# Kernel optimization log

Measured on AMD Instinct MI355X. Metric: run time of the kernel, lower is better.

The kernel has to match this reference:

```python
import jax, jax.numpy as jnp
import numpy as np

B, T, D, H, R = 16, 2048, 512, 1024, 16


def setup_inputs() -> dict:
    key = jax.random.key(0)
    ks = jax.random.split(key, 8)
    s = lambda d: 1.0 / np.sqrt(d)
    return {
        "x": jax.random.normal(ks[0], (B, T, D), jnp.float32),
        "Wx": jax.random.normal(ks[1], (D, H), jnp.float32) * s(D),
        "Wh": jax.random.normal(ks[2], (H, H), jnp.float32) * s(H),
        "Wq": jax.random.normal(ks[3], (D, R), jnp.float32) * s(D),
        "Wk": jax.random.normal(ks[4], (D, R), jnp.float32) * s(D),
        "Wv": jax.random.normal(ks[5], (D, H), jnp.float32) * s(D),
        "Wd": jax.random.normal(ks[6], (D, 1), jnp.float32) * s(D),
        "b": jnp.zeros((H,), jnp.float32),
        "bd": jnp.ones((1,), jnp.float32),
    }


def reference(x, Wx, Wh, Wq, Wk, Wv, Wd, b, bd):
    """DREAM fast-weight RNN.

    Per step: decay lambda_t = sigmoid(x_t Wd + bd)  (B,1)
              F_t = lambda_t * F_{t-1} + v_t k_t^T   (B,H,R) outer-product memory
              r_t = F_t q_t                          (B,H)   fast-weight read
              h_t = tanh(x_t Wx + h_{t-1} Wh + r_t + b)
    """
    Bsz = x.shape[0]
    Hd, Rk = Wv.shape[1], Wq.shape[1]
    # Precompute all time-parallel projections once (big GEMMs outside the scan).
    q = jnp.einsum('btd,dr->btr', x, Wq)            # (B,T,R)
    k = jnp.einsum('btd,dr->btr', x, Wk)            # (B,T,R)
    v = jnp.einsum('btd,dh->bth', x, Wv)            # (B,T,H)
    lam = jax.nn.sigmoid(jnp.einsum('btd,do->bto', x, Wd) + bd)  # (B,T,1)
    xw = jnp.einsum('btd,dh->bth', x, Wx)           # (B,T,H)

    h0 = jnp.zeros((Bsz, Hd), x.dtype)
    F0 = jnp.zeros((Bsz, Hd, Rk), x.dtype)

    def step(carry, inp):
        h, F = carry
        q_t, k_t, v_t, lam_t, xw_t = inp
        F = lam_t[:, :, None] * F + v_t[:, :, None] * k_t[:, None, :]  # (B,H,R)
        read = jnp.einsum('bhr,br->bh', F, q_t)
        h = jnp.tanh(xw_t + h @ Wh + read + b)
        return (h, F), h

    # scan over time axis
    inps = (q.transpose(1, 0, 2), k.transpose(1, 0, 2), v.transpose(1, 0, 2),
            lam.transpose(1, 0, 2), xw.transpose(1, 0, 2))
    (h_fin, F_fin), hs = jax.lax.scan(step, (h0, F0), inps)
    output = hs.transpose(1, 0, 2)  # (B,T,H)
    return output, h_fin, F_fin
```

## Files before the change

kernel.cpp:

```cpp
#include <hip/hip_runtime.h>
#include <math.h>

#define Bc 16
#define Tc 2048
#define Dc 512
#define Hc 1024
#define Rc 16

__global__ __launch_bounds__(256) void gemm_xw(const float* __restrict__ X,
                                               const float* __restrict__ W,
                                               float* __restrict__ out)
{
    __shared__ float As[16][128];
    __shared__ float Bs[16][64];
    const int tid = threadIdx.x;
    const int m0 = blockIdx.x * 128;
    const int n0 = blockIdx.y * 64;
    const int tx = tid & 15, ty = tid >> 4;
    const int am = tid >> 2, ak = (tid & 3) * 4;
    const int bk = tid >> 4, bn = (tid & 15) * 4;
    float acc[8][4] = {};
    for (int k0 = 0; k0 < 512; k0 += 16) {
        if (k0) __syncthreads();
        float4 a0 = *(const float4*)&X[(size_t)(m0 + am) * 512 + k0 + ak];
        float4 a1 = *(const float4*)&X[(size_t)(m0 + am + 64) * 512 + k0 + ak];
        float4 bv = *(const float4*)&W[(size_t)(k0 + bk) * 1024 + n0 + bn];
        As[ak + 0][am] = a0.x; As[ak + 1][am] = a0.y;
        As[ak + 2][am] = a0.z; As[ak + 3][am] = a0.w;
        As[ak + 0][am + 64] = a1.x; As[ak + 1][am + 64] = a1.y;
        As[ak + 2][am + 64] = a1.z; As[ak + 3][am + 64] = a1.w;
        *(float4*)&Bs[bk][bn] = bv;
        __syncthreads();
        #pragma unroll
        for (int kk = 0; kk < 16; ++kk) {
            float4 x0 = *(const float4*)&As[kk][ty * 8];
            float4 x1 = *(const float4*)&As[kk][ty * 8 + 4];
            float4 y  = *(const float4*)&Bs[kk][tx * 4];
            float a[8] = {x0.x, x0.y, x0.z, x0.w, x1.x, x1.y, x1.z, x1.w};
            float bb[4] = {y.x, y.y, y.z, y.w};
            #pragma unroll
            for (int i = 0; i < 8; ++i)
                #pragma unroll
                for (int j = 0; j < 4; ++j)
                    acc[i][j] += a[i] * bb[j];
        }
    }
    #pragma unroll
    for (int i = 0; i < 8; ++i) {
        float4 r;
        r.x = acc[i][0]; r.y = acc[i][1]; r.z = acc[i][2]; r.w = acc[i][3];
        *(float4*)&out[(size_t)(m0 + ty * 8 + i) * 1024 + n0 + tx * 4] = r;
    }
}

__global__ __launch_bounds__(256) void qkl_kernel(const float* __restrict__ X,
    const float* __restrict__ Wq, const float* __restrict__ Wk,
    const float* __restrict__ Wd, const float* __restrict__ bd,
    float* __restrict__ q, float* __restrict__ k, float* __restrict__ lam)
{
    __shared__ float xs[8 * 512];
    const int tid = threadIdx.x;
    const size_t row0 = (size_t)blockIdx.x * 8;
    #pragma unroll
    for (int c = 0; c < 4; ++c) {
        int f = (c * 256 + tid) * 4;
        *(float4*)&xs[f] = *(const float4*)&X[row0 * 512 + f];
    }
    __syncthreads();
    for (int t = tid; t < 264; t += 256) {
        int r = t / 33, c = t - r * 33;
        const float* xr = &xs[r * 512];
        const float* Wp; int ldw;
        if (c < 16)      { Wp = Wq + c;        ldw = 16; }
        else if (c < 32) { Wp = Wk + (c - 16); ldw = 16; }
        else             { Wp = Wd;            ldw = 1;  }
        float s = 0.f;
        for (int kk = 0; kk < 512; ++kk) s += xr[kk] * Wp[(size_t)kk * ldw];
        if (c < 16)      q[(row0 + r) * 16 + c] = s;
        else if (c < 32) k[(row0 + r) * 16 + (c - 16)] = s;
        else             lam[row0 + r] = 1.f / (1.f + expf(-(s + bd[0])));
    }
}

__global__ __launch_bounds__(256, 1) void rec_fused(
    const float* __restrict__ Wh, const float* __restrict__ qg,
    const float* __restrict__ kg, const float* __restrict__ vg,
    const float* __restrict__ lamg, const float* __restrict__ bias,
    float* __restrict__ out0, float* __restrict__ hfin,
    float* __restrict__ Ffin, float* __restrict__ hbuf)
{
    __shared__ float hs[4 * 1280];
    __shared__ float red2[2][256];
    __shared__ float pre_lds[2][64];
    __shared__ float F_lds[64][17];

    const int tid = threadIdx.x;
    const int w = blockIdx.x;
    const int sl = w & 63, g = w >> 6;
    const int c0 = sl * 16;
    const int kp = tid >> 2;
    const int cg = tid & 3;
    const int wv = tid >> 6;

    float wr[64];
    #pragma unroll
    for (int i = 0; i < 16; ++i) {
        float4 w4 = *(const float4*)&Wh[(size_t)(kp * 16 + i) * 1024 + c0 + cg * 4];
        wr[i * 4 + 0] = w4.x; wr[i * 4 + 1] = w4.y;
        wr[i * 4 + 2] = w4.z; wr[i * 4 + 3] = w4.w;
    }

    const int j64 = tid & 63;
    const int sb = j64 >> 4, scol = j64 & 15;
    const int sbg = g * 4 + sb;
    const bool isScan = (tid >= 192);
    const bool isFin  = (tid < 64);
    float bias_r = 0.f;
    float4 pq[4], pk4[4];
    float plam = 0.f, pv = 0.f, pxw = 0.f;
    if (isScan) {
        bias_r = bias[c0 + scol];
        #pragma unroll
        for (int r = 0; r < 16; ++r) F_lds[j64][r] = 0.f;
        const size_t row = (size_t)sbg * Tc;
        plam = lamg[row];
        pv   = vg[row * Hc + c0 + scol];
        pxw  = out0[row * Hc + c0 + scol];
        const float* qp = qg + row * 16;
        const float* kpp = kg + row * 16;
        #pragma unroll
        for (int r4 = 0; r4 < 4; ++r4) {
            pq[r4]  = *(const float4*)(qp + r4 * 4);
            pk4[r4] = *(const float4*)(kpp + r4 * 4);
        }
    }

    for (int t = 0; t < Tc; ++t) {
        const int buf = t & 1;
        float* h_rd = hbuf + (t & 1) * (Bc * Hc) + g * 4096;
        float* h_wr = hbuf + ((t + 1) & 1) * (Bc * Hc) + g * 4096;
        const float off_r = ((t >> 1) & 1) ? 4.0f : 0.0f;
        const float off_w = (((t + 1) >> 1) & 1) ? 4.0f : 0.0f;

        if (isScan) {
            float rd = 0.f;
            #pragma unroll
            for (int r4 = 0; r4 < 4; ++r4) {
                float f0 = F_lds[j64][r4 * 4 + 0];
                float f1 = F_lds[j64][r4 * 4 + 1];
                float f2 = F_lds[j64][r4 * 4 + 2];
                float f3 = F_lds[j64][r4 * 4 + 3];
                f0 = plam * f0 + pv * pk4[r4].x; rd += f0 * pq[r4].x;
                f1 = plam * f1 + pv * pk4[r4].y; rd += f1 * pq[r4].y;
                f2 = plam * f2 + pv * pk4[r4].z; rd += f2 * pq[r4].z;
                f3 = plam * f3 + pv * pk4[r4].w; rd += f3 * pq[r4].w;
                F_lds[j64][r4 * 4 + 0] = f0;
                F_lds[j64][r4 * 4 + 1] = f1;
                F_lds[j64][r4 * 4 + 2] = f2;
                F_lds[j64][r4 * 4 + 3] = f3;
            }
            pre_lds[buf][j64] = pxw + rd + bias_r;
            if (t == Tc - 1) {
                #pragma unroll
                for (int r = 0; r < 16; ++r)
                    Ffin[((size_t)sbg * Hc + c0 + scol) * 16 + r] = F_lds[j64][r];
            } else {
                const size_t row = (size_t)sbg * Tc + (t + 1);
                plam = lamg[row];
                pv   = vg[row * Hc + c0 + scol];
                pxw  = out0[row * Hc + c0 + scol];
                const float* qp = qg + row * 16;
                const float* kpp = kg + row * 16;
                #pragma unroll
                for (int r4 = 0; r4 < 4; ++r4) {
                    pq[r4]  = *(const float4*)(qp + r4 * 4);
                    pk4[r4] = *(const float4*)(kpp + r4 * 4);
                }
            }
        }

        {
            const int chunk = tid >> 2, coff = (tid & 3) * 4;
            float* base = &hs[chunk * 20 + coff];
            if (t > 0) {
                const float lo = off_r - 1.5f, hi = off_r + 1.5f;
                const float* p0 = h_rd + tid * 4;
                const float* p1 = p0 + 1024;
                const float* p2 = p0 + 2048;
                const float* p3 = p0 + 3072;
                float4 r0, r1, r2, r3;
                while (1) {
                    asm volatile(
                        "global_load_dwordx4 %0, %4, off sc0 sc1\n\t"
                        "global_load_dwordx4 %1, %5, off sc0 sc1\n\t"
                        "global_load_dwordx4 %2, %6, off sc0 sc1\n\t"
                        "global_load_dwordx4 %3, %7, off sc0 sc1\n\t"
                        "s_waitcnt vmcnt(0)"
                        : "=&v"(r0), "=&v"(r1), "=&v"(r2), "=&v"(r3)
                        : "v"(p0), "v"(p1), "v"(p2), "v"(p3)
                        : "memory");
                    bool ok = r0.x > lo && r0.x < hi && r0.y > lo && r0.y < hi
                           && r0.z > lo && r0.z < hi && r0.w > lo && r0.w < hi
                           && r1.x > lo && r1.x < hi && r1.y > lo && r1.y < hi
                           && r1.z > lo && r1.z < hi && r1.w > lo && r1.w < hi
                           && r2.x > lo && r2.x < hi && r2.y > lo && r2.y < hi
                           && r2.z > lo && r2.z < hi && r2.w > lo && r2.w < hi
                           && r3.x > lo && r3.x < hi && r3.y > lo && r3.y < hi
                           && r3.z > lo && r3.z < hi && r3.w > lo && r3.w < hi;
                    if (ok) break;
                }
                r0.x -= off_r; r0.y -= off_r; r0.z -= off_r; r0.w -= off_r;
                r1.x -= off_r; r1.y -= off_r; r1.z -= off_r; r1.w -= off_r;
                r2.x -= off_r; r2.y -= off_r; r2.z -= off_r; r2.w -= off_r;
                r3.x -= off_r; r3.y -= off_r; r3.z -= off_r; r3.w -= off_r;
                *(float4*)(base + 0 * 1280) = r0;
                *(float4*)(base + 1 * 1280) = r1;
                *(float4*)(base + 2 * 1280) = r2;
                *(float4*)(base + 3 * 1280) = r3;
            } else {
                float4 z = {0.f, 0.f, 0.f, 0.f};
                *(float4*)(base + 0 * 1280) = z;
                *(float4*)(base + 1 * 1280) = z;
                *(float4*)(base + 2 * 1280) = z;
                *(float4*)(base + 3 * 1280) = z;
            }
        }
        __syncthreads();

        float acc[16];
        #pragma unroll
        for (int z = 0; z < 16; ++z) acc[z] = 0.f;
        #pragma unroll
        for (int b = 0; b < 4; ++b) {
            const float* hb = &hs[b * 1280 + kp * 20];
            #pragma unroll
            for (int e = 0; e < 4; ++e) {
                float4 h4 = *(const float4*)(hb + e * 4);
                #pragma unroll
                for (int j = 0; j < 4; ++j)
                    acc[j * 4 + b] += h4.x * wr[(e * 4 + 0) * 4 + j]
                                    + h4.y * wr[(e * 4 + 1) * 4 + j]
                                    + h4.z * wr[(e * 4 + 2) * 4 + j]
                                    + h4.w * wr[(e * 4 + 3) * 4 + j];
            }
        }

        #pragma unroll
        for (int z = 0; z < 16; ++z) {
            float s = acc[z];
            s += __shfl_xor(s, 4);
            s += __shfl_xor(s, 8);
            s += __shfl_xor(s, 16);
            s += __shfl_xor(s, 32);
            acc[z] = s;
        }
        if (j64 < 4) {
            #pragma unroll
            for (int j = 0; j < 4; ++j) {
                float4 r4;
                r4.x = acc[j * 4 + 0]; r4.y = acc[j * 4 + 1];
                r4.z = acc[j * 4 + 2]; r4.w = acc[j * 4 + 3];
                *(float4*)&red2[buf][wv * 64 + (j64 * 4 + j) * 4] = r4;
            }
        }
        __syncthreads();

        if (isFin) {
            const int fb = tid >> 4, fcol = tid & 15;
            float tot = pre_lds[buf][tid];
            #pragma unroll
            for (int ww = 0; ww < 4; ++ww)
                tot += red2[buf][ww * 64 + fcol * 4 + fb];
            float hv = tanhf(tot);
            float sv = hv + off_w;
            float* hp = h_wr + fb * 1024 + c0 + fcol;
            asm volatile(
                "global_store_dword %0, %1, off sc0 sc1"
                :: "v"(hp), "v"(sv) : "memory");
            size_t oidx = ((size_t)(g * 4 + fb) * Tc + t) * Hc + c0 + fcol;
            out0[oidx] = hv;
            if (t == Tc - 1) hfin[(size_t)(g * 4 + fb) * Hc + c0 + fcol] = hv;
        }
    }
}

extern "C" void kernel_launch(void* const* d_in, const int* in_sizes, int n_in,
                              void* d_out, int out_size, void* d_ws, size_t ws_size,
                              hipStream_t stream)
{
    const float* x    = (const float*)d_in[0];
    const float* Wx   = (const float*)d_in[1];
    const float* Wh   = (const float*)d_in[2];
    const float* Wq   = (const float*)d_in[3];
    const float* Wk   = (const float*)d_in[4];
    const float* Wv   = (const float*)d_in[5];
    const float* Wd   = (const float*)d_in[6];
    const float* bias = (const float*)d_in[7];
    const float* bd   = (const float*)d_in[8];

    float* out0 = (float*)d_out;
    float* hfin = out0 + (size_t)Bc * Tc * Hc;
    float* Ffin = hfin + (size_t)Bc * Hc;

    float* wsf  = (float*)d_ws;
    float* v    = wsf;
    float* q    = v + (size_t)Bc * Tc * Hc;
    float* k    = q + (size_t)Bc * Tc * Rc;
    float* lam  = k + (size_t)Bc * Tc * Rc;
    float* hbuf = lam + (size_t)Bc * Tc;

    hipMemsetAsync(hbuf, 0x7F, 2 * (size_t)Bc * Hc * sizeof(float), stream);

    dim3 gg(256, 16);
    gemm_xw<<<gg, 256, 0, stream>>>(x, Wx, out0);
    gemm_xw<<<gg, 256, 0, stream>>>(x, Wv, v);
    qkl_kernel<<<4096, 256, 0, stream>>>(x, Wq, Wk, Wd, bd, q, k, lam);
    rec_fused<<<256, 256, 0, stream>>>(Wh, q, k, v, lam, bias,
                                       out0, hfin, Ffin, hbuf);
}
```

Before: 8.838 ms.

## Add a dedicated fifth wavefront for fast-weight scan and finalize, keep F in registers

The recurrent kernel grows from 256 to 320 threads per block. A separate fifth wavefront now runs the fast-weight memory update, the read, the tanh finalize and the global h store. The four compute wavefronts only do the h·Wh matvec. The F state moves from LDS into per-thread registers, and the pre-activation is passed in a register instead of through LDS. This removes the scan and finalize work from the matvec wavefronts and drops LDS traffic for F, which should shorten the per-step critical path. In exchange the block has one more wave to synchronise, and the finalize now runs on the same wave as the next step's scan, which could serialise them.

```diff
diff --git a/kernel.cpp b/kernel.cpp
--- a/kernel.cpp
+++ b/kernel.cpp
@@ -82,7 +82,7 @@
     }
 }
 
-__global__ __launch_bounds__(256, 1) void rec_fused(
+__global__ __launch_bounds__(320, 1) void rec_fused(
     const float* __restrict__ Wh, const float* __restrict__ qg,
     const float* __restrict__ kg, const float* __restrict__ vg,
     const float* __restrict__ lamg, const float* __restrict__ bias,
@@ -91,42 +91,45 @@
 {
     __shared__ float hs[4 * 1280];
     __shared__ float red2[2][256];
-    __shared__ float pre_lds[2][64];
-    __shared__ float F_lds[64][17];
 
     const int tid = threadIdx.x;
     const int w = blockIdx.x;
     const int sl = w & 63, g = w >> 6;
     const int c0 = sl * 16;
-    const int kp = tid >> 2;
+    const bool isC = (tid < 256);
+    const bool isS = (tid >= 256);
+    const int kp = (tid >> 2) & 63;
     const int cg = tid & 3;
     const int wv = tid >> 6;
+    const int j64 = tid & 63;
+    const int sb = j64 >> 4, scol = j64 & 15;
+    const int sbg = g * 4 + sb;
 
     float wr[64];
     #pragma unroll
     for (int i = 0; i < 16; ++i) {
-        float4 w4 = *(const float4*)&Wh[(size_t)(kp * 16 + i) * 1024 + c0 + cg * 4];
-        wr[i * 4 + 0] = w4.x; wr[i * 4 + 1] = w4.y;
-        wr[i * 4 + 2] = w4.z; wr[i * 4 + 3] = w4.w;
-    }
-
-    const int j64 = tid & 63;
-    const int sb = j64 >> 4, scol = j64 & 15;
-    const int sbg = g * 4 + sb;
-    const bool isScan = (tid >= 192);
-    const bool isFin  = (tid < 64);
-    float bias_r = 0.f;
+        if (isC) {
+            float4 w4 = *(const float4*)&Wh[(size_t)(kp * 16 + i) * 1024 + c0 + cg * 4];
+            wr[i * 4 + 0] = w4.x; wr[i * 4 + 1] = w4.y;
+            wr[i * 4 + 2] = w4.z; wr[i * 4 + 3] = w4.w;
+        } else {
+            wr[i * 4 + 0] = 0.f; wr[i * 4 + 1] = 0.f;
+            wr[i * 4 + 2] = 0.f; wr[i * 4 + 3] = 0.f;
+        }
+    }
+
+    float F[16];
+    #pragma unroll
+    for (int r = 0; r < 16; ++r) F[r] = 0.f;
+    float bias_r = 0.f, plam = 0.f, pv = 0.f, pxw = 0.f;
     float4 pq[4], pk4[4];
-    float plam = 0.f, pv = 0.f, pxw = 0.f;
-    if (isScan) {
+    if (isS) {
         bias_r = bias[c0 + scol];
-        #pragma unroll
-        for (int r = 0; r < 16; ++r) F_lds[j64][r] = 0.f;
         const size_t row = (size_t)sbg * Tc;
         plam = lamg[row];
         pv   = vg[row * Hc + c0 + scol];
         pxw  = out0[row * Hc + c0 + scol];
-        const float* qp = qg + row * 16;
+        const float* qp  = qg + row * 16;
         const float* kpp = kg + row * 16;
         #pragma unroll
         for (int r4 = 0; r4 < 4; ++r4) {
@@ -142,34 +145,31 @@
         const float off_r = ((t >> 1) & 1) ? 4.0f : 0.0f;
         const float off_w = (((t + 1) >> 1) & 1) ? 4.0f : 0.0f;
 
-        if (isScan) {
+        float pre_val = 0.f;
+        if (isS) {
             float rd = 0.f;
             #pragma unroll
             for (int r4 = 0; r4 < 4; ++r4) {
-                float f0 = F_lds[j64][r4 * 4 + 0];
-                float f1 = F_lds[j64][r4 * 4 + 1];
-                float f2 = F_lds[j64][r4 * 4 + 2];
-                float f3 = F_lds[j64][r4 * 4 + 3];
+                float f0 = F[r4 * 4 + 0], f1 = F[r4 * 4 + 1];
+                float f2 = F[r4 * 4 + 2], f3 = F[r4 * 4 + 3];
                 f0 = plam * f0 + pv * pk4[r4].x; rd += f0 * pq[r4].x;
                 f1 = plam * f1 + pv * pk4[r4].y; rd += f1 * pq[r4].y;
                 f2 = plam * f2 + pv * pk4[r4].z; rd += f2 * pq[r4].z;
                 f3 = plam * f3 + pv * pk4[r4].w; rd += f3 * pq[r4].w;
-                F_lds[j64][r4 * 4 + 0] = f0;
-                F_lds[j64][r4 * 4 + 1] = f1;
-                F_lds[j64][r4 * 4 + 2] = f2;
-                F_lds[j64][r4 * 4 + 3] = f3;
-            }
-            pre_lds[buf][j64] = pxw + rd + bias_r;
+                F[r4 * 4 + 0] = f0; F[r4 * 4 + 1] = f1;
+                F[r4 * 4 + 2] = f2; F[r4 * 4 + 3] = f3;
+            }
+            pre_val = pxw + rd + bias_r;
             if (t == Tc - 1) {
                 #pragma unroll
                 for (int r = 0; r < 16; ++r)
-                    Ffin[((size_t)sbg * Hc + c0 + scol) * 16 + r] = F_lds[j64][r];
+                    Ffin[((size_t)sbg * Hc + c0 + scol) * 16 + r] = F[r];
             } else {
                 const size_t row = (size_t)sbg * Tc + (t + 1);
                 plam = lamg[row];
                 pv   = vg[row * Hc + c0 + scol];
                 pxw  = out0[row * Hc + c0 + scol];
-                const float* qp = qg + row * 16;
+                const float* qp  = qg + row * 16;
                 const float* kpp = kg + row * 16;
                 #pragma unroll
                 for (int r4 = 0; r4 < 4; ++r4) {
@@ -179,7 +179,7 @@
             }
         }
 
-        {
+        if (isC) {
             const int chunk = tid >> 2, coff = (tid & 3) * 4;
             float* base = &hs[chunk * 20 + coff];
             if (t > 0) {
@@ -227,59 +227,59 @@
         }
         __syncthreads();
 
-        float acc[16];
-        #pragma unroll
-        for (int z = 0; z < 16; ++z) acc[z] = 0.f;
-        #pragma unroll
-        for (int b = 0; b < 4; ++b) {
-            const float* hb = &hs[b * 1280 + kp * 20];
-            #pragma unroll
-            for (int e = 0; e < 4; ++e) {
-                float4 h4 = *(const float4*)(hb + e * 4);
-                #pragma unroll
-                for (int j = 0; j < 4; ++j)
-                    acc[j * 4 + b] += h4.x * wr[(e * 4 + 0) * 4 + j]
-                                    + h4.y * wr[(e * 4 + 1) * 4 + j]
-                                    + h4.z * wr[(e * 4 + 2) * 4 + j]
-                                    + h4.w * wr[(e * 4 + 3) * 4 + j];
-            }
-        }
-
-        #pragma unroll
-        for (int z = 0; z < 16; ++z) {
-            float s = acc[z];
-            s += __shfl_xor(s, 4);
-            s += __shfl_xor(s, 8);
-            s += __shfl_xor(s, 16);
-            s += __shfl_xor(s, 32);
-            acc[z] = s;
-        }
-        if (j64 < 4) {
-            #pragma unroll
-            for (int j = 0; j < 4; ++j) {
-                float4 r4;
-                r4.x = acc[j * 4 + 0]; r4.y = acc[j * 4 + 1];
-                r4.z = acc[j * 4 + 2]; r4.w = acc[j * 4 + 3];
-                *(float4*)&red2[buf][wv * 64 + (j64 * 4 + j) * 4] = r4;
+        if (isC) {
+            float acc[16];
+            #pragma unroll
+            for (int z = 0; z < 16; ++z) acc[z] = 0.f;
+            #pragma unroll
+            for (int b = 0; b < 4; ++b) {
+                const float* hb = &hs[b * 1280 + kp * 20];
+                #pragma unroll
+                for (int e = 0; e < 4; ++e) {
+                    float4 h4 = *(const float4*)(hb + e * 4);
+                    #pragma unroll
+                    for (int j = 0; j < 4; ++j)
+                        acc[j * 4 + b] += h4.x * wr[(e * 4 + 0) * 4 + j]
+                                        + h4.y * wr[(e * 4 + 1) * 4 + j]
+                                        + h4.z * wr[(e * 4 + 2) * 4 + j]
+                                        + h4.w * wr[(e * 4 + 3) * 4 + j];
+                }
+            }
+            #pragma unroll
+            for (int z = 0; z < 16; ++z) {
+                float s = acc[z];
+                s += __shfl_xor(s, 4);
+                s += __shfl_xor(s, 8);
+                s += __shfl_xor(s, 16);
+                s += __shfl_xor(s, 32);
+                acc[z] = s;
+            }
+            if (j64 < 4) {
+                #pragma unroll
+                for (int j = 0; j < 4; ++j) {
+                    float4 r4;
+                    r4.x = acc[j * 4 + 0]; r4.y = acc[j * 4 + 1];
+                    r4.z = acc[j * 4 + 2]; r4.w = acc[j * 4 + 3];
+                    *(float4*)&red2[buf][wv * 64 + (j64 * 4 + j) * 4] = r4;
+                }
             }
         }
         __syncthreads();
 
-        if (isFin) {
-            const int fb = tid >> 4, fcol = tid & 15;
-            float tot = pre_lds[buf][tid];
+        if (isS) {
+            float tot = pre_val;
             #pragma unroll
             for (int ww = 0; ww < 4; ++ww)
-                tot += red2[buf][ww * 64 + fcol * 4 + fb];
+                tot += red2[buf][ww * 64 + scol * 4 + sb];
             float hv = tanhf(tot);
             float sv = hv + off_w;
-            float* hp = h_wr + fb * 1024 + c0 + fcol;
+            float* hp = h_wr + sb * 1024 + c0 + scol;
             asm volatile(
                 "global_store_dword %0, %1, off sc0 sc1"
                 :: "v"(hp), "v"(sv) : "memory");
-            size_t oidx = ((size_t)(g * 4 + fb) * Tc + t) * Hc + c0 + fcol;
+            size_t oidx = ((size_t)sbg * Tc + t) * Hc + c0 + scol;
             out0[oidx] = hv;
-            if (t == Tc - 1) hfin[(size_t)(g * 4 + fb) * Hc + c0 + fcol] = hv;
+            if (t == Tc - 1) hfin[(size_t)sbg * Hc + c0 + scol] = hv;
         }
     }
 }
@@ -315,6 +315,6 @@
     gemm_xw<<<gg, 256, 0, stream>>>(x, Wx, out0);
     gemm_xw<<<gg, 256, 0, stream>>>(x, Wv, v);
     qkl_kernel<<<4096, 256, 0, stream>>>(x, Wq, Wk, Wd, bd, q, k, lam);
-    rec_fused<<<256, 256, 0, stream>>>(Wh, q, k, v, lam, bias,
+    rec_fused<<<256, 320, 0, stream>>>(Wh, q, k, v, lam, bias,
                                        out0, hfin, Ffin, hbuf);
 }
```

Measured after the change: 13.03 ms. 1.47x slower.

## Repartition recurrence into 8 batch groups and add XCC-aware cache-coherent polling

Applied to the files above, without the earlier changes.

The recurrence is regrouped into 8 groups of 2 batches with 32 columns per block, where it was 4 groups of 4 batches with 16 columns. Each block now holds 128 Wh registers per thread and reads only 2 batch rows of h per step. Each block records which XCC it runs on in a table. When the producer block of a chunk is on the same XCC, the consumer polls with sc0-only loads to avoid system-level coherent traffic, and falls back to sc0 sc1 after 64 failed tries. This risks higher register pressure and depends on the reported XCC id being correct for L2-level coherence.

```diff
diff --git a/kernel.cpp b/kernel.cpp
--- a/kernel.cpp
+++ b/kernel.cpp
@@ -87,46 +87,73 @@
     const float* __restrict__ kg, const float* __restrict__ vg,
     const float* __restrict__ lamg, const float* __restrict__ bias,
     float* __restrict__ out0, float* __restrict__ hfin,
-    float* __restrict__ Ffin, float* __restrict__ hbuf)
+    float* __restrict__ Ffin, float* __restrict__ hbuf,
+    int* __restrict__ xcc_tab)
 {
-    __shared__ float hs[4 * 1280];
+    __shared__ float hs[2 * 1152];
     __shared__ float red2[2][256];
     __shared__ float pre_lds[2][64];
     __shared__ float F_lds[64][17];
 
     const int tid = threadIdx.x;
-    const int w = blockIdx.x;
-    const int sl = w & 63, g = w >> 6;
-    const int c0 = sl * 16;
-    const int kp = tid >> 2;
-    const int cg = tid & 3;
+    const int bid = blockIdx.x;
+    const int g = bid & 7, sl = bid >> 3;
+    const int c0 = sl * 32;
+    const int kp = tid >> 3;
+    const int cu = tid & 7;
     const int wv = tid >> 6;
 
-    float wr[64];
+    const int my_xcc = __builtin_amdgcn_s_getreg(63508) & 0xF;
+    if (tid == 0) {
+        int val = my_xcc + 1;
+        int* tp = xcc_tab + bid;
+        asm volatile("global_store_dword %0, %1, off sc0 sc1"
+                     :: "v"(tp), "v"(val) : "memory");
+    }
+
+    float wr[128];
     #pragma unroll
-    for (int i = 0; i < 16; ++i) {
-        float4 w4 = *(const float4*)&Wh[(size_t)(kp * 16 + i) * 1024 + c0 + cg * 4];
+    for (int i = 0; i < 32; ++i) {
+        float4 w4 = *(const float4*)&Wh[(size_t)(kp * 32 + i) * 1024 + c0 + cu * 4];
         wr[i * 4 + 0] = w4.x; wr[i * 4 + 1] = w4.y;
         wr[i * 4 + 2] = w4.z; wr[i * 4 + 3] = w4.w;
     }
 
+    const int sb_ = tid >> 7;
+    const int f   = (tid & 127) * 8;
+    float* stage_base = &hs[sb_ * 1152 + (f >> 5) * 36 + (f & 31)];
+
+    int fastf;
+    {
+        const int prod_bid = (f >> 5) * 8 + g;
+        const int* tp = xcc_tab + prod_bid;
+        int tv;
+        for (;;) {
+            asm volatile("global_load_dword %0, %1, off sc0 sc1\n\t"
+                         "s_waitcnt vmcnt(0)"
+                         : "=&v"(tv) : "v"(tp) : "memory");
+            if (tv != -1) break;
+        }
+        fastf = ((tv - 1) == my_xcc) ? 1 : 0;
+    }
+
     const int j64 = tid & 63;
-    const int sb = j64 >> 4, scol = j64 & 15;
-    const int sbg = g * 4 + sb;
+    const int fb = j64 >> 5, fci = j64 & 31;
+    const int bg = g * 2 + fb;
     const bool isScan = (tid >= 192);
     const bool isFin  = (tid < 64);
-    float bias_r = 0.f;
+
+    float bias_r = 0.f, plam = 0.f, pv = 0.f, pxw = 0.f;
     float4 pq[4], pk4[4];
-    float plam = 0.f, pv = 0.f, pxw = 0.f;
     if (isScan) {
-        bias_r = bias[c0 + scol];
+        bias_r = bias[c0 + fci];
         #pragma unroll
         for (int r = 0; r < 16; ++r) F_lds[j64][r] = 0.f;
-        const size_t row = (size_t)sbg * Tc;
+        const size_t row = (size_t)bg * Tc;
         plam = lamg[row];
-        pv   = vg[row * Hc + c0 + scol];
-        pxw  = out0[row * Hc + c0 + scol];
-        const float* qp = qg + row * 16;
+        pv   = vg[row * Hc + c0 + fci];
+        pxw  = out0[row * Hc + c0 + fci];
+        const float* qp  = qg + row * 16;
         const float* kpp = kg + row * 16;
         #pragma unroll
         for (int r4 = 0; r4 < 4; ++r4) {
@@ -137,8 +164,8 @@
 
     for (int t = 0; t < Tc; ++t) {
         const int buf = t & 1;
-        float* h_rd = hbuf + (t & 1) * (Bc * Hc) + g * 4096;
-        float* h_wr = hbuf + ((t + 1) & 1) * (Bc * Hc) + g * 4096;
+        float* h_rd = hbuf + (t & 1) * (16 * 1024) + g * 2048;
+        float* h_wr = hbuf + ((t + 1) & 1) * (16 * 1024) + g * 2048;
         const float off_r = ((t >> 1) & 1) ? 4.0f : 0.0f;
         const float off_w = (((t + 1) >> 1) & 1) ? 4.0f : 0.0f;
 
@@ -163,13 +190,13 @@
             if (t == Tc - 1) {
                 #pragma unroll
                 for (int r = 0; r < 16; ++r)
-                    Ffin[((size_t)sbg * Hc + c0 + scol) * 16 + r] = F_lds[j64][r];
+                    Ffin[((size_t)bg * Hc + c0 + fci) * 16 + r] = F_lds[j64][r];
             } else {
-                const size_t row = (size_t)sbg * Tc + (t + 1);
+                const size_t row = (size_t)bg * Tc + (t + 1);
                 plam = lamg[row];
-                pv   = vg[row * Hc + c0 + scol];
-                pxw  = out0[row * Hc + c0 + scol];
-                const float* qp = qg + row * 16;
+                pv   = vg[row * Hc + c0 + fci];
+                pxw  = out0[row * Hc + c0 + fci];
+                const float* qp  = qg + row * 16;
                 const float* kpp = kg + row * 16;
                 #pragma unroll
                 for (int r4 = 0; r4 < 4; ++r4) {
@@ -179,107 +206,97 @@
             }
         }
 
-        {
-            const int chunk = tid >> 2, coff = (tid & 3) * 4;
-            float* base = &hs[chunk * 20 + coff];
-            if (t > 0) {
-                const float lo = off_r - 1.5f, hi = off_r + 1.5f;
-                const float* p0 = h_rd + tid * 4;
-                const float* p1 = p0 + 1024;
-                const float* p2 = p0 + 2048;
-                const float* p3 = p0 + 3072;
-                float4 r0, r1, r2, r3;
-                while (1) {
+        if (t > 0) {
+            const float lo = off_r - 1.5f, hi = off_r + 1.5f;
+            const float* p0 = h_rd + sb_ * 1024 + f;
+            const float* p1 = p0 + 4;
+            float4 r0, r1;
+            int tries = 0;
+            for (;;) {
+                if (fastf) {
                     asm volatile(
-                        "global_load_dwordx4 %0, %4, off sc0 sc1\n\t"
-                        "global_load_dwordx4 %1, %5, off sc0 sc1\n\t"
-                        "global_load_dwordx4 %2, %6, off sc0 sc1\n\t"
-                        "global_load_dwordx4 %3, %7, off sc0 sc1\n\t"
+                        "global_load_dwordx4 %0, %2, off sc0\n\t"
+                        "global_load_dwordx4 %1, %3, off sc0\n\t"
                         "s_waitcnt vmcnt(0)"
-                        : "=&v"(r0), "=&v"(r1), "=&v"(r2), "=&v"(r3)
-                        : "v"(p0), "v"(p1), "v"(p2), "v"(p3)
-                        : "memory");
-                    bool ok = r0.x > lo && r0.x < hi && r0.y > lo && r0.y < hi
-                           && r0.z > lo && r0.z < hi && r0.w > lo && r0.w < hi
-                           && r1.x > lo && r1.x < hi && r1.y > lo && r1.y < hi
-                           && r1.z > lo && r1.z < hi && r1.w > lo && r1.w < hi
-                           && r2.x > lo && r2.x < hi && r2.y > lo && r2.y < hi
-                           && r2.z > lo && r2.z < hi && r2.w > lo && r2.w < hi
-                           && r3.x > lo && r3.x < hi && r3.y > lo && r3.y < hi
-                           && r3.z > lo && r3.z < hi && r3.w > lo && r3.w < hi;
-                    if (ok) break;
+                        : "=&v"(r0), "=&v"(r1)
+                        : "v"(p0), "v"(p1) : "memory");
+                } else {
+                    asm volatile(
+                        "global_load_dwordx4 %0, %2, off sc0 sc1\n\t"
+                        "global_load_dwordx4 %1, %3, off sc0 sc1\n\t"
+                        "s_waitcnt vmcnt(0)"
+                        : "=&v"(r0), "=&v"(r1)
+                        : "v"(p0), "v"(p1) : "memory");
                 }
-                r0.x -= off_r; r0.y -= off_r; r0.z -= off_r; r0.w -= off_r;
-                r1.x -= off_r; r1.y -= off_r; r1.z -= off_r; r1.w -= off_r;
-                r2.x -= off_r; r2.y -= off_r; r2.z -= off_r; r2.w -= off_r;
-                r3.x -= off_r; r3.y -= off_r; r3.z -= off_r; r3.w -= off_r;
-                *(float4*)(base + 0 * 1280) = r0;
-                *(float4*)(base + 1 * 1280) = r1;
-                *(float4*)(base + 2 * 1280) = r2;
-                *(float4*)(base + 3 * 1280) = r3;
-            } else {
-                float4 z = {0.f, 0.f, 0.f, 0.f};
-                *(float4*)(base + 0 * 1280) = z;
-                *(float4*)(base + 1 * 1280) = z;
-                *(float4*)(base + 2 * 1280) = z;
-                *(float4*)(base + 3 * 1280) = z;
+                bool ok = r0.x > lo && r0.x < hi && r0.y > lo && r0.y < hi
+                       && r0.z > lo && r0.z < hi && r0.w > lo && r0.w < hi
+                       && r1.x > lo && r1.x < hi && r1.y > lo && r1.y < hi
+                       && r1.z > lo && r1.z < hi && r1.w > lo && r1.w < hi;
+                if (ok) break;
+                if (fastf && ++tries > 64) fastf = 0;
             }
+            r0.x -= off_r; r0.y -= off_r; r0.z -= off_r; r0.w -= off_r;
+            r1.x -= off_r; r1.y -= off_r; r1.z -= off_r; r1.w -= off_r;
+            *(float4*)(stage_base)     = r0;
+            *(float4*)(stage_base + 4) = r1;
+        } else {
+            float4 z = {0.f, 0.f, 0.f, 0.f};
+            *(float4*)(stage_base)     = z;
+            *(float4*)(stage_base + 4) = z;
         }
         __syncthreads();
 
-        float acc[16];
-        #pragma unroll
-        for (int z = 0; z < 16; ++z) acc[z] = 0.f;
-        #pragma unroll
-        for (int b = 0; b < 4; ++b) {
-            const float* hb = &hs[b * 1280 + kp * 20];
+        float acc[8];
+        #pragma unroll
+        for (int z = 0; z < 8; ++z) acc[z] = 0.f;
+        #pragma unroll
+        for (int bb = 0; bb < 2; ++bb) {
+            const float* hb = &hs[bb * 1152 + kp * 36];
             #pragma unroll
-            for (int e = 0; e < 4; ++e) {
-                float4 h4 = *(const float4*)(hb + e * 4);
+            for (int i = 0; i < 8; ++i) {
+                float4 h4 = *(const float4*)(hb + i * 4);
                 #pragma unroll
                 for (int j = 0; j < 4; ++j)
-                    acc[j * 4 + b] += h4.x * wr[(e * 4 + 0) * 4 + j]
-                                    + h4.y * wr[(e * 4 + 1) * 4 + j]
-                                    + h4.z * wr[(e * 4 + 2) * 4 + j]
-                                    + h4.w * wr[(e * 4 + 3) * 4 + j];
+                    acc[j * 2 + bb] += h4.x * wr[(i * 4 + 0) * 4 + j]
+                                     + h4.y * wr[(i * 4 + 1) * 4 + j]
+                                     + h4.z * wr[(i * 4 + 2) * 4 + j]
+                                     + h4.w * wr[(i * 4 + 3) * 4 + j];
             }
         }
 
         #pragma unroll
-        for (int z = 0; z < 16; ++z) {
+        for (int z = 0; z < 8; ++z) {
             float s = acc[z];
-            s += __shfl_xor(s, 4);
             s += __shfl_xor(s, 8);
             s += __shfl_xor(s, 16);
             s += __shfl_xor(s, 32);
             acc[z] = s;
         }
-        if (j64 < 4) {
-            #pragma unroll
-            for (int j = 0; j < 4; ++j) {
-                float4 r4;
-                r4.x = acc[j * 4 + 0]; r4.y = acc[j * 4 + 1];
-                r4.z = acc[j * 4 + 2]; r4.w = acc[j * 4 + 3];
-                *(float4*)&red2[buf][wv * 64 + (j64 * 4 + j) * 4] = r4;
-            }
+        if (j64 < 8) {
+            float4 ra, rb;
+            ra.x = acc[0]; ra.y = acc[1]; ra.z = acc[2]; ra.w = acc[3];
+            rb.x = acc[4]; rb.y = acc[5]; rb.z = acc[6]; rb.w = acc[7];
+            *(float4*)&red2[buf][wv * 64 + j64 * 8]     = ra;
+            *(float4*)&red2[buf][wv * 64 + j64 * 8 + 4] = rb;
         }
         __syncthreads();
 
         if (isFin) {
-            const int fb = tid >> 4, fcol = tid & 15;
-            float tot = pre_lds[buf][tid];
+            const int cu_f = fci >> 2, jf = fci & 3;
+            const int z = jf * 2 + fb;
+            float tot = pre_lds[buf][j64];
             #pragma unroll
             for (int ww = 0; ww < 4; ++ww)
-                tot += red2[buf][ww * 64 + fcol * 4 + fb];
+                tot += red2[buf][ww * 64 + cu_f * 8 + z];
             float hv = tanhf(tot);
             float sv = hv + off_w;
-            float* hp = h_wr + fb * 1024 + c0 + fcol;
+            float* hp = h_wr + fb * 1024 + c0 + fci;
             asm volatile(
                 "global_store_dword %0, %1, off sc0 sc1"
                 :: "v"(hp), "v"(sv) : "memory");
-            size_t oidx = ((size_t)(g * 4 + fb) * Tc + t) * Hc + c0 + fcol;
+            size_t oidx = ((size_t)bg * Tc + t) * Hc + c0 + fci;
             out0[oidx] = hv;
-            if (t == Tc - 1) hfin[(size_t)(g * 4 + fb) * Hc + c0 + fcol] = hv;
+            if (t == Tc - 1) hfin[(size_t)bg * Hc + c0 + fci] = hv;
         }
     }
 }
@@ -308,13 +325,15 @@
     float* k    = q + (size_t)Bc * Tc * Rc;
     float* lam  = k + (size_t)Bc * Tc * Rc;
     float* hbuf = lam + (size_t)Bc * Tc;
+    int*   xcc  = (int*)(hbuf + 2 * (size_t)Bc * Hc);
 
     hipMemsetAsync(hbuf, 0x7F, 2 * (size_t)Bc * Hc * sizeof(float), stream);
+    hipMemsetAsync(xcc, 0xFF, 256 * sizeof(int), stream);
 
     dim3 gg(256, 16);
     gemm_xw<<<gg, 256, 0, stream>>>(x, Wx, out0);
     gemm_xw<<<gg, 256, 0, stream>>>(x, Wv, v);
     qkl_kernel<<<4096, 256, 0, stream>>>(x, Wq, Wk, Wd, bd, q, k, lam);
     rec_fused<<<256, 256, 0, stream>>>(Wh, q, k, v, lam, bias,
-                                       out0, hfin, Ffin, hbuf);
+                                       out0, hfin, Ffin, hbuf, xcc);
 }
```

After: 7.531 ms. 14.8% less time.
